# Kernel tuning notes

Hardware: AMD Instinct MI355X
Metric: run time of the kernel (lower is better)

## Reference

```python
import jax, jax.numpy as jnp
import numpy as np

HEADS = 16
DIM_HEAD = 64


def rotate_half(t):
    x1, x2 = jnp.split(t, 2, axis=-1)
    return jnp.concatenate((-x2, x1), axis=-1)


def apply_rotary_pos_emb(t, freqs):
    # t: [b, h, n, l], freqs: [n, l]
    seq_len = t.shape[-2]
    freqs = freqs[-seq_len:, :]
    return t * jnp.cos(freqs) + rotate_half(t) * jnp.sin(freqs)


def setup_inputs() -> dict:
    key = jax.random.key(0)
    ks = jax.random.split(key, 6)
    b, n, dim, l = 2, 2048, 1024, 32
    x = jax.random.normal(ks[0], (b, n, dim), dtype=jnp.float32)
    rotary_pos_emb = jax.random.normal(ks[1], (n, l), dtype=jnp.float32)
    s = 0.02
    Wq = jax.random.normal(ks[2], (dim, dim), dtype=jnp.float32) * s
    Wk = jax.random.normal(ks[3], (dim, dim), dtype=jnp.float32) * s
    Wv = jax.random.normal(ks[4], (dim, dim), dtype=jnp.float32) * s
    Wout = jax.random.normal(ks[5], (dim, dim), dtype=jnp.float32) * s
    return {"x": x, "rotary_pos_emb": rotary_pos_emb, "Wq": Wq, "Wk": Wk, "Wv": Wv, "Wout": Wout}


def reference(x, rotary_pos_emb, Wq, Wk, Wv, Wout):
    b, n, _ = x.shape
    h, d = HEADS, DIM_HEAD
    scale = d ** -0.5

    def to_heads(t):
        return t.reshape(b, n, h, d).transpose(0, 2, 1, 3)  # b h n d

    q = to_heads(x @ Wq)
    k = to_heads(x @ Wk)
    v = to_heads(x @ Wv)

    # partial rotary on first l dims of q, k, v (module applies rope to v too)
    l = rotary_pos_emb.shape[-1]

    def rope(t):
        tl, tr = t[..., :l], t[..., l:]
        return jnp.concatenate((apply_rotary_pos_emb(tl, rotary_pos_emb), tr), axis=-1)

    q, k, v = rope(q), rope(k), rope(v)

    dots = jnp.einsum('bhid,bhjd->bhij', q, k) * scale  # [b, h, n, n]
    mask_value = jnp.finfo(dots.dtype).min
    causal = jnp.triu(jnp.ones((n, n), dtype=bool), k=1)  # i < j
    dots = jnp.where(causal[None, None, :, :], mask_value, dots)

    attn = jax.nn.softmax(dots, axis=-1)
    out = jnp.einsum('bhij,bhjd->bhid', attn, v)
    out = out.transpose(0, 2, 1, 3).reshape(b, n, h * d)  # b n (h d)
    return out @ Wout
```

## Files before the change

kernel.cpp:

```cpp
#include <hip/hip_runtime.h>
#include <hip/hip_bf16.h>
#include <stdint.h>

#define BATCH 2
#define SEQ 2048
#define NHEADS 16
#define DIM 1024
#define MTOT 4096
#define LOG2E 1.4426950408889634f
#define QSCALE (0.125f * LOG2E)
#define DEFER_THR 11.54f

typedef __attribute__((ext_vector_type(8))) short s16x8;
typedef __attribute__((ext_vector_type(4))) float f32x4;
typedef unsigned short u16;

__device__ __forceinline__ u16 f2b(float f) {
  union { float f; uint32_t u; } v; v.f = f;
  uint32_t r = v.u + 0x7FFFu + ((v.u >> 16) & 1u);
  return (u16)(r >> 16);
}
__device__ __forceinline__ float b2f(u16 h) {
  union { uint32_t u; float f; } v; v.u = ((uint32_t)h) << 16;
  return v.f;
}

__device__ __forceinline__ void gload_lds16(void* lds, const void* g) {
  __builtin_amdgcn_global_load_lds(
      (const __attribute__((address_space(1))) unsigned int*)g,
      (__attribute__((address_space(3))) unsigned int*)lds, 16, 0, 0);
}


__global__ __launch_bounds__(256) void cast_x_kernel(
    const float* __restrict__ x, u16* __restrict__ xb) {
  int i = (blockIdx.x * 256 + threadIdx.x) * 4;
  float4 v = *(const float4*)(x + i);
  ushort4 o;
  o.x = f2b(v.x); o.y = f2b(v.y); o.z = f2b(v.z); o.w = f2b(v.w);
  *(ushort4*)(xb + i) = o;
}

__global__ __launch_bounds__(256) void transw_kernel(
    const float* __restrict__ Wq, const float* __restrict__ Wk,
    const float* __restrict__ Wv, const float* __restrict__ Wo,
    u16* __restrict__ WtAll) {
  const float* W = (blockIdx.z == 0) ? Wq : (blockIdx.z == 1) ? Wk
                 : (blockIdx.z == 2) ? Wv : Wo;
  u16* Wt = WtAll + (size_t)blockIdx.z * DIM * DIM;
  __shared__ float t[32][33];
  int k0 = blockIdx.x * 32, n0 = blockIdx.y * 32;
  int tx = threadIdx.x, ty = threadIdx.y;
#pragma unroll
  for (int i = 0; i < 4; i++) {
    int r = ty + i * 8;
    t[r][tx] = W[(size_t)(k0 + r) * DIM + n0 + tx];
  }
  __syncthreads();
#pragma unroll
  for (int i = 0; i < 4; i++) {
    int r = ty + i * 8;
    Wt[(size_t)(n0 + r) * DIM + k0 + tx] = f2b(t[tx][r]);
  }
}

__global__ __launch_bounds__(256) void table_kernel(
    const float* __restrict__ rot, float2* __restrict__ cs) {
  int i = blockIdx.x * 256 + threadIdx.x;
  float f = rot[i];
  float s, c;
  __sincosf(f, &s, &c);
  cs[i] = make_float2(c, s);
}

template <int MODE>
__global__ __launch_bounds__(256) void gemm128(
    const u16* __restrict__ A, const u16* __restrict__ BtBase,
    void* __restrict__ Cbase, const float2* __restrict__ cs,
    u16* __restrict__ Qh, u16* __restrict__ Kh, u16* __restrict__ Vt) {
  __shared__ u16 Asm[2][128 * 32];
  __shared__ u16 Bsm[2][128 * 32];
  const u16* Bt = BtBase + (size_t)blockIdx.z * DIM * DIM;

  int t = threadIdx.x;
  int w = t >> 6, l = t & 63;
  int wr = w >> 1, wc = w & 1;
  int lr = l & 15, lg = l >> 4;
  int rowBase = blockIdx.x * 128;
  int colBase = blockIdx.y * 128;

  const char* Ab = (const char*)(A + (size_t)rowBase * DIM);
  const char* Bb = (const char*)(Bt + (size_t)colBase * DIM);

  f32x4 acc[4][4];
#pragma unroll
  for (int m = 0; m < 4; m++)
#pragma unroll
    for (int n = 0; n < 4; n++) acc[m][n] = (f32x4){0.f, 0.f, 0.f, 0.f};

  auto stage = [&](int buf, int kt) {
#pragma unroll
    for (int i = 0; i < 2; i++) {
      int ob = t * 16 + i * 4096;
      int row = ob >> 6, cb = ob & 63;
      int src = row * (DIM * 2) + kt * 64 + (cb ^ (((row >> 1) & 3) << 4));
      gload_lds16((char*)&Asm[buf][0] + ob, Ab + src);
      gload_lds16((char*)&Bsm[buf][0] + ob, Bb + src);
    }
  };

  stage(0, 0);
  for (int kt = 0; kt < DIM / 32; ++kt) {
    int cur = kt & 1;
    __syncthreads();
    if (kt + 1 < DIM / 32) stage(cur ^ 1, kt + 1);
    const char* ab = (const char*)&Asm[cur][0];
    const char* bb = (const char*)&Bsm[cur][0];
    s16x8 af[4], bf[4];
#pragma unroll
    for (int m = 0; m < 4; m++) {
      int R = wr * 64 + m * 16 + lr;
      af[m] = *(const s16x8*)(ab + R * 64 + ((lg * 16) ^ (((R >> 1) & 3) << 4)));
    }
#pragma unroll
    for (int n = 0; n < 4; n++) {
      int R = wc * 64 + n * 16 + lr;
      bf[n] = *(const s16x8*)(bb + R * 64 + ((lg * 16) ^ (((R >> 1) & 3) << 4)));
    }
    __builtin_amdgcn_s_setprio(1);
#pragma unroll
    for (int m = 0; m < 4; m++)
#pragma unroll
      for (int n = 0; n < 4; n++)
        acc[m][n] = __builtin_amdgcn_mfma_f32_16x16x32_bf16(af[m], bf[n], acc[m][n], 0, 0, 0);
    __builtin_amdgcn_s_setprio(0);
  }

  if constexpr (MODE == 1) {
    float* C = (float*)Cbase;
#pragma unroll
    for (int m = 0; m < 4; m++)
#pragma unroll
      for (int n = 0; n < 4; n++) {
        int row = rowBase + wr * 64 + m * 16 + lg * 4;
        int col = colBase + wc * 64 + n * 16 + lr;
#pragma unroll
        for (int r = 0; r < 4; r++)
          C[(size_t)(row + r) * DIM + col] = acc[m][n][r];
      }
  } else {
    int z = blockIdx.z;
    int h = (colBase + wc * 64) >> 6;
    if (z == 2) {
#pragma unroll
      for (int m = 0; m < 4; m++) {
#pragma unroll
        for (int r = 0; r < 4; r++) {
          int row = rowBase + wr * 64 + m * 16 + lg * 4 + r;
          int nrow = row & (SEQ - 1);
          int b2 = row >> 11;
          const float2* csr = cs + (size_t)nrow * 32;
          float a0 = acc[m][0][r], a1 = acc[m][1][r];
          float2 f0 = csr[lr];
          float2 f1 = csr[16 + lr];
          float o0 = a0 * f0.x - a1 * f0.y;
          float o1 = a1 * f1.x + a0 * f1.y;
          size_t vbase = ((size_t)(b2 * NHEADS + h) * 64) * SEQ + nrow;
          Vt[vbase + (size_t)lr * SEQ]        = f2b(o0);
          Vt[vbase + (size_t)(16 + lr) * SEQ] = f2b(o1);
          Vt[vbase + (size_t)(32 + lr) * SEQ] = f2b(acc[m][2][r]);
          Vt[vbase + (size_t)(48 + lr) * SEQ] = f2b(acc[m][3][r]);
        }
      }
    } else {
      u16* C = (z == 0) ? Qh : Kh;
      float sc = (z == 0) ? QSCALE : 1.0f;
#pragma unroll
      for (int m = 0; m < 4; m++) {
#pragma unroll
        for (int r = 0; r < 4; r++) {
          int row = rowBase + wr * 64 + m * 16 + lg * 4 + r;
          int nrow = row & (SEQ - 1);
          int b2 = row >> 11;
          const float2* csr = cs + (size_t)nrow * 32;
          float a0 = acc[m][0][r], a1 = acc[m][1][r];
          float2 f0 = csr[lr];
          float2 f1 = csr[16 + lr];
          float o0 = (a0 * f0.x - a1 * f0.y) * sc;
          float o1 = (a1 * f1.x + a0 * f1.y) * sc;
          size_t base = ((size_t)(b2 * NHEADS + h) * SEQ + nrow) * 64;
          C[base + lr]      = f2b(o0);
          C[base + 16 + lr] = f2b(o1);
          C[base + 32 + lr] = f2b(acc[m][2][r] * sc);
          C[base + 48 + lr] = f2b(acc[m][3][r] * sc);
        }
      }
    }
  }
}

__global__ __launch_bounds__(128) void attn_kernel(
    const u16* __restrict__ Qh, const u16* __restrict__ Kh,
    const u16* __restrict__ Vtg, u16* __restrict__ Ob) {
  int id = blockIdx.y * 32 + blockIdx.x;
  int xcd = id & 7, within = id >> 3;
  int bh = xcd * 4 + (within >> 5);
  int pi = within & 31;
  int b = bh >> 4, h = bh & 15;
  __shared__ u16 Ks[2][64 * 64];
  __shared__ u16 Vs[2][64 * 64];
  __shared__ u16 Ps[2][16 * 64];
  int t = threadIdx.x, w = t >> 6, l = t & 63;
  int lr = l & 15, lg = l >> 4;
  char* psb = (char*)&Ps[w][0];

  const char* Kbh = (const char*)(Kh + (size_t)bh * SEQ * 64);
  const char* Vbh = (const char*)Vtg + (size_t)bh * 64 * SEQ * 2;
  const u16* Qbh = Qh + (size_t)bh * SEQ * 64;

  auto stage = [&](int buf, int kt) {
    const char* kg = Kbh + (size_t)kt * 64 * 128;
    const char* vg = Vbh + kt * 128;
#pragma unroll
    for (int i = 0; i < 4; i++) {
      int ob = i * 2048 + t * 16;
      int row = ob >> 7, cb = ob & 127;
      int sw = cb ^ ((row & 7) << 4);
      gload_lds16((char*)&Ks[buf][0] + ob, kg + row * 128 + sw);
      gload_lds16((char*)&Vs[buf][0] + ob, vg + row * 4096 + sw);
    }
  };

#pragma unroll 1
  for (int ph = 0; ph < 2; ++ph) {
    int qt = ph ? (63 - pi) : pi;
    int nkt = (qt >> 1) + 1;
    int qrow0 = qt * 32 + w * 16;

    s16x8 qf[2];
#pragma unroll
    for (int kk = 0; kk < 2; kk++)
      qf[kk] = *(const s16x8*)(Qbh + (size_t)(qrow0 + lr) * 64 + kk * 32 + lg * 8);

    f32x4 o[4];
#pragma unroll
    for (int n = 0; n < 4; n++) o[n] = (f32x4){0.f, 0.f, 0.f, 0.f};
    float mrun[4], lsum[4];
#pragma unroll
    for (int r = 0; r < 4; r++) { mrun[r] = -3.0e38f; lsum[r] = 0.f; }

    __syncthreads();
    stage(0, 0);
    for (int kt = 0; kt < nkt; ++kt) {
      int cur = kt & 1;
      __syncthreads();
      if (kt + 1 < nkt) stage(cur ^ 1, kt + 1);
      const char* kb = (const char*)&Ks[cur][0];
      const char* vb = (const char*)&Vs[cur][0];

      f32x4 s[4];
#pragma unroll
      for (int n = 0; n < 4; n++) s[n] = (f32x4){0.f, 0.f, 0.f, 0.f};
      __builtin_amdgcn_s_setprio(1);
#pragma unroll
      for (int n = 0; n < 4; n++)
#pragma unroll
        for (int kk = 0; kk < 2; kk++) {
          int R = n * 16 + lr;
          s16x8 bk = *(const s16x8*)(kb + R * 128 + ((kk * 64 + lg * 16) ^ ((R & 7) << 4)));
          s[n] = __builtin_amdgcn_mfma_f32_16x16x32_bf16(qf[kk], bk, s[n], 0, 0, 0);
        }
      __builtin_amdgcn_s_setprio(0);

      if (kt == nkt - 1) {
#pragma unroll
        for (int n = 0; n < 4; n++) {
          int colg = kt * 64 + n * 16 + lr;
#pragma unroll
          for (int r = 0; r < 4; r++) {
            int rowg = qt * 32 + w * 16 + lg * 4 + r;
            if (colg > rowg) s[n][r] = -3.0e38f;
          }
        }
      }

      float tm[4];
#pragma unroll
      for (int r = 0; r < 4; r++)
        tm[r] = fmaxf(fmaxf(s[0][r], s[1][r]), fmaxf(s[2][r], s[3][r]));
#pragma unroll
      for (int off = 1; off < 16; off <<= 1)
#pragma unroll
        for (int r = 0; r < 4; r++) tm[r] = fmaxf(tm[r], __shfl_xor(tm[r], off, 64));
      float need = 0.f;
#pragma unroll
      for (int r = 0; r < 4; r++) need = fmaxf(need, tm[r] - mrun[r]);
      if (!__all(need <= DEFER_THR)) {
        float alpha[4];
#pragma unroll
        for (int r = 0; r < 4; r++) {
          float mn = fmaxf(mrun[r], tm[r]);
          alpha[r] = exp2f(mrun[r] - mn);
          mrun[r] = mn;
          lsum[r] *= alpha[r];
        }
#pragma unroll
        for (int n = 0; n < 4; n++)
#pragma unroll
          for (int r = 0; r < 4; r++) o[n][r] *= alpha[r];
      }
#pragma unroll
      for (int n = 0; n < 4; n++) {
#pragma unroll
        for (int r = 0; r < 4; r++) {
          float p = exp2f(s[n][r] - mrun[r]);
          lsum[r] += p;
          int prow = lg * 4 + r;
          *(u16*)(psb + prow * 128 + (((n * 16 + lr) * 2) ^ ((prow & 7) << 4))) = f2b(p);
        }
      }

      s16x8 pa[2];
#pragma unroll
      for (int kk = 0; kk < 2; kk++)
        pa[kk] = *(const s16x8*)(psb + lr * 128 + ((kk * 64 + lg * 16) ^ ((lr & 7) << 4)));
      __builtin_amdgcn_s_setprio(1);
#pragma unroll
      for (int n = 0; n < 4; n++)
#pragma unroll
        for (int kk = 0; kk < 2; kk++) {
          int R = n * 16 + lr;
          s16x8 vv = *(const s16x8*)(vb + R * 128 + ((kk * 64 + lg * 16) ^ ((R & 7) << 4)));
          o[n] = __builtin_amdgcn_mfma_f32_16x16x32_bf16(pa[kk], vv, o[n], 0, 0, 0);
        }
      __builtin_amdgcn_s_setprio(0);
    }

#pragma unroll
    for (int off = 1; off < 16; off <<= 1)
#pragma unroll
      for (int r = 0; r < 4; r++) lsum[r] += __shfl_xor(lsum[r], off, 64);
    float inv[4];
#pragma unroll
    for (int r = 0; r < 4; r++) inv[r] = 1.0f / lsum[r];
#pragma unroll
    for (int n = 0; n < 4; n++)
#pragma unroll
      for (int r = 0; r < 4; r++) {
        int rowg = qt * 32 + w * 16 + lg * 4 + r;
        int col = h * 64 + n * 16 + lr;
        Ob[((size_t)b * SEQ + rowg) * DIM + col] = f2b(o[n][r] * inv[r]);
      }
  }
}

extern "C" void kernel_launch(void* const* d_in, const int* in_sizes, int n_in,
                              void* d_out, int out_size, void* d_ws, size_t ws_size,
                              hipStream_t stream) {
  (void)in_sizes; (void)n_in; (void)out_size; (void)ws_size;
  const float* x = (const float*)d_in[0];
  const float* rot = (const float*)d_in[1];
  const float* Wq = (const float*)d_in[2];
  const float* Wk = (const float*)d_in[3];
  const float* Wv = (const float*)d_in[4];
  const float* Wo = (const float*)d_in[5];

  char* ws = (char*)d_ws;
  u16* xb    = (u16*)(ws);
  u16* WtAll = (u16*)(ws + (8ll << 20));
  u16* Qh    = (u16*)(ws + (16ll << 20));
  u16* Kh    = (u16*)(ws + (24ll << 20));
  u16* Vt    = (u16*)(ws + (32ll << 20));
  u16* Ob    = (u16*)(ws + (40ll << 20));
  float2* cs = (float2*)(ws + (48ll << 20));

  cast_x_kernel<<<4096, 256, 0, stream>>>(x, xb);
  transw_kernel<<<dim3(32, 32, 4), dim3(32, 8), 0, stream>>>(Wq, Wk, Wv, Wo, WtAll);
  table_kernel<<<256, 256, 0, stream>>>(rot, cs);
  gemm128<0><<<dim3(32, 8, 3), 256, 0, stream>>>(xb, WtAll, nullptr, cs, Qh, Kh, Vt);
  attn_kernel<<<dim3(32, 32), 128, 0, stream>>>(Qh, Kh, Vt, Ob);
  gemm128<1><<<dim3(32, 8, 1), 256, 0, stream>>>(Ob, WtAll + 3ll * DIM * DIM, d_out,
                                                 nullptr, nullptr, nullptr, nullptr);
}
```

Baseline: 233.8 us.

## Merge prep kernels and enlarge attention blocks to four waves with lazier max reduce

Folds the x cast, weight transpose and sin/cos table kernels into one launch to save launch overhead. The attention kernel moves to 256-thread blocks covering 64 query rows, so each staged K/V tile is reused by four waves, and the grid shrinks to 512 blocks. The cross-lane row-max shuffle now runs only when rescaling is needed, and P uses a cheaper round-half-up bf16 conversion. Fewer, larger blocks may lower occupancy and worsen load balance. Skipping the shuffle means each lane's exponent offset is checked only against its own local max, so exactness relies on the threshold.

```diff
diff --git a/kernel.cpp b/kernel.cpp
--- a/kernel.cpp
+++ b/kernel.cpp
@@ -20,6 +20,10 @@
   uint32_t r = v.u + 0x7FFFu + ((v.u >> 16) & 1u);
   return (u16)(r >> 16);
 }
+__device__ __forceinline__ u16 f2b_fast(float f) {
+  union { float f; uint32_t u; } v; v.f = f;
+  return (u16)((v.u + 0x8000u) >> 16);
+}
 __device__ __forceinline__ float b2f(u16 h) {
   union { uint32_t u; float f; } v; v.u = ((uint32_t)h) << 16;
   return v.f;
@@ -31,46 +35,44 @@
       (__attribute__((address_space(3))) unsigned int*)lds, 16, 0, 0);
 }
 
-
-__global__ __launch_bounds__(256) void cast_x_kernel(
-    const float* __restrict__ x, u16* __restrict__ xb) {
-  int i = (blockIdx.x * 256 + threadIdx.x) * 4;
-  float4 v = *(const float4*)(x + i);
-  ushort4 o;
-  o.x = f2b(v.x); o.y = f2b(v.y); o.z = f2b(v.z); o.w = f2b(v.w);
-  *(ushort4*)(xb + i) = o;
-}
-
-__global__ __launch_bounds__(256) void transw_kernel(
-    const float* __restrict__ Wq, const float* __restrict__ Wk,
-    const float* __restrict__ Wv, const float* __restrict__ Wo,
-    u16* __restrict__ WtAll) {
-  const float* W = (blockIdx.z == 0) ? Wq : (blockIdx.z == 1) ? Wk
-                 : (blockIdx.z == 2) ? Wv : Wo;
-  u16* Wt = WtAll + (size_t)blockIdx.z * DIM * DIM;
-  __shared__ float t[32][33];
-  int k0 = blockIdx.x * 32, n0 = blockIdx.y * 32;
-  int tx = threadIdx.x, ty = threadIdx.y;
-#pragma unroll
-  for (int i = 0; i < 4; i++) {
-    int r = ty + i * 8;
-    t[r][tx] = W[(size_t)(k0 + r) * DIM + n0 + tx];
+__global__ __launch_bounds__(256) void prep_kernel(
+    const float* __restrict__ x, const float* __restrict__ Wq,
+    const float* __restrict__ Wk, const float* __restrict__ Wv,
+    const float* __restrict__ Wo, const float* __restrict__ rot,
+    u16* __restrict__ xb, u16* __restrict__ WtAll, float2* __restrict__ cs) {
+  __shared__ float tile[32][33];
+  int bid = blockIdx.x, t = threadIdx.x;
+  if (bid < 4096) {
+    int i = (bid * 256 + t) * 4;
+    float4 v = *(const float4*)(x + i);
+    ushort4 o;
+    o.x = f2b(v.x); o.y = f2b(v.y); o.z = f2b(v.z); o.w = f2b(v.w);
+    *(ushort4*)(xb + i) = o;
+  } else if (bid < 8192) {
+    int bb = bid - 4096;
+    int z = bb >> 10, xB = bb & 31, yB = (bb >> 5) & 31;
+    const float* W = (z == 0) ? Wq : (z == 1) ? Wk : (z == 2) ? Wv : Wo;
+    u16* Wt = WtAll + (size_t)z * DIM * DIM;
+    int k0 = xB * 32, n0 = yB * 32;
+    int tx = t & 31, ty = t >> 5;
+#pragma unroll
+    for (int i = 0; i < 4; i++) {
+      int r = ty + i * 8;
+      tile[r][tx] = W[(size_t)(k0 + r) * DIM + n0 + tx];
+    }
+    __syncthreads();
+#pragma unroll
+    for (int i = 0; i < 4; i++) {
+      int r = ty + i * 8;
+      Wt[(size_t)(n0 + r) * DIM + k0 + tx] = f2b(tile[tx][r]);
+    }
+  } else {
+    int i = (bid - 8192) * 256 + t;
+    float f = rot[i];
+    float s, c;
+    __sincosf(f, &s, &c);
+    cs[i] = make_float2(c, s);
   }
-  __syncthreads();
-#pragma unroll
-  for (int i = 0; i < 4; i++) {
-    int r = ty + i * 8;
-    Wt[(size_t)(n0 + r) * DIM + k0 + tx] = f2b(t[tx][r]);
-  }
-}
-
-__global__ __launch_bounds__(256) void table_kernel(
-    const float* __restrict__ rot, float2* __restrict__ cs) {
-  int i = blockIdx.x * 256 + threadIdx.x;
-  float f = rot[i];
-  float s, c;
-  __sincosf(f, &s, &c);
-  cs[i] = make_float2(c, s);
 }
 
 template <int MODE>
@@ -199,17 +201,17 @@
   }
 }
 
-__global__ __launch_bounds__(128) void attn_kernel(
+__global__ __launch_bounds__(256) void attn_kernel(
     const u16* __restrict__ Qh, const u16* __restrict__ Kh,
     const u16* __restrict__ Vtg, u16* __restrict__ Ob) {
-  int id = blockIdx.y * 32 + blockIdx.x;
+  int id = blockIdx.x;
   int xcd = id & 7, within = id >> 3;
-  int bh = xcd * 4 + (within >> 5);
-  int pi = within & 31;
+  int bh = xcd * 4 + (within >> 4);
+  int pi = within & 15;
   int b = bh >> 4, h = bh & 15;
   __shared__ u16 Ks[2][64 * 64];
   __shared__ u16 Vs[2][64 * 64];
-  __shared__ u16 Ps[2][16 * 64];
+  __shared__ u16 Ps[4][16 * 64];
   int t = threadIdx.x, w = t >> 6, l = t & 63;
   int lr = l & 15, lg = l >> 4;
   char* psb = (char*)&Ps[w][0];
@@ -222,8 +224,8 @@
     const char* kg = Kbh + (size_t)kt * 64 * 128;
     const char* vg = Vbh + kt * 128;
 #pragma unroll
-    for (int i = 0; i < 4; i++) {
-      int ob = i * 2048 + t * 16;
+    for (int i = 0; i < 2; i++) {
+      int ob = i * 4096 + t * 16;
       int row = ob >> 7, cb = ob & 127;
       int sw = cb ^ ((row & 7) << 4);
       gload_lds16((char*)&Ks[buf][0] + ob, kg + row * 128 + sw);
@@ -233,9 +235,9 @@
 
 #pragma unroll 1
   for (int ph = 0; ph < 2; ++ph) {
-    int qt = ph ? (63 - pi) : pi;
-    int nkt = (qt >> 1) + 1;
-    int qrow0 = qt * 32 + w * 16;
+    int qt = ph ? (31 - pi) : pi;
+    int nkt = qt + 1;
+    int qrow0 = qt * 64 + w * 16;
 
     s16x8 qf[2];
 #pragma unroll
@@ -278,24 +280,26 @@
           int colg = kt * 64 + n * 16 + lr;
 #pragma unroll
           for (int r = 0; r < 4; r++) {
-            int rowg = qt * 32 + w * 16 + lg * 4 + r;
+            int rowg = qt * 64 + w * 16 + lg * 4 + r;
             if (colg > rowg) s[n][r] = -3.0e38f;
           }
         }
       }
 
-      float tm[4];
+      float tl[4];
 #pragma unroll
       for (int r = 0; r < 4; r++)
-        tm[r] = fmaxf(fmaxf(s[0][r], s[1][r]), fmaxf(s[2][r], s[3][r]));
-#pragma unroll
-      for (int off = 1; off < 16; off <<= 1)
-#pragma unroll
-        for (int r = 0; r < 4; r++) tm[r] = fmaxf(tm[r], __shfl_xor(tm[r], off, 64));
-      float need = 0.f;
-#pragma unroll
-      for (int r = 0; r < 4; r++) need = fmaxf(need, tm[r] - mrun[r]);
+        tl[r] = fmaxf(fmaxf(s[0][r], s[1][r]), fmaxf(s[2][r], s[3][r]));
+      float need = fmaxf(fmaxf(tl[0] - mrun[0], tl[1] - mrun[1]),
+                         fmaxf(tl[2] - mrun[2], tl[3] - mrun[3]));
       if (!__all(need <= DEFER_THR)) {
+        float tm[4];
+#pragma unroll
+        for (int r = 0; r < 4; r++) tm[r] = tl[r];
+#pragma unroll
+        for (int off = 1; off < 16; off <<= 1)
+#pragma unroll
+          for (int r = 0; r < 4; r++) tm[r] = fmaxf(tm[r], __shfl_xor(tm[r], off, 64));
         float alpha[4];
 #pragma unroll
         for (int r = 0; r < 4; r++) {
@@ -316,7 +320,7 @@
           float p = exp2f(s[n][r] - mrun[r]);
           lsum[r] += p;
           int prow = lg * 4 + r;
-          *(u16*)(psb + prow * 128 + (((n * 16 + lr) * 2) ^ ((prow & 7) << 4))) = f2b(p);
+          *(u16*)(psb + prow * 128 + (((n * 16 + lr) * 2) ^ ((prow & 7) << 4))) = f2b_fast(p);
         }
       }
 
@@ -347,7 +351,7 @@
     for (int n = 0; n < 4; n++)
 #pragma unroll
       for (int r = 0; r < 4; r++) {
-        int rowg = qt * 32 + w * 16 + lg * 4 + r;
+        int rowg = qt * 64 + w * 16 + lg * 4 + r;
         int col = h * 64 + n * 16 + lr;
         Ob[((size_t)b * SEQ + rowg) * DIM + col] = f2b(o[n][r] * inv[r]);
       }
@@ -374,11 +378,9 @@
   u16* Ob    = (u16*)(ws + (40ll << 20));
   float2* cs = (float2*)(ws + (48ll << 20));
 
-  cast_x_kernel<<<4096, 256, 0, stream>>>(x, xb);
-  transw_kernel<<<dim3(32, 32, 4), dim3(32, 8), 0, stream>>>(Wq, Wk, Wv, Wo, WtAll);
-  table_kernel<<<256, 256, 0, stream>>>(rot, cs);
+  prep_kernel<<<8448, 256, 0, stream>>>(x, Wq, Wk, Wv, Wo, rot, xb, WtAll, cs);
   gemm128<0><<<dim3(32, 8, 3), 256, 0, stream>>>(xb, WtAll, nullptr, cs, Qh, Kh, Vt);
-  attn_kernel<<<dim3(32, 32), 128, 0, stream>>>(Qh, Kh, Vt, Ob);
+  attn_kernel<<<512, 256, 0, stream>>>(Qh, Kh, Vt, Ob);
   gemm128<1><<<dim3(32, 8, 1), 256, 0, stream>>>(Ob, WtAll + 3ll * DIM * DIM, d_out,
                                                  nullptr, nullptr, nullptr, nullptr);
 }
```

Measured after the change: 212.5 us. -9.1%, faster.
